# Kernel tuning notes

Hardware: AMD Instinct MI355X
Metric: run time of the kernel (lower is better)

The kernel has to match this reference:

```python
import jax, jax.numpy as jnp
import numpy as np

T, H, I, E, K = 2048, 1024, 768, 16, 4

def setup_inputs() -> dict:
    key = jax.random.key(0)
    k1, k2, k3, k4, k5 = jax.random.split(key, 5)
    hidden_states = jax.random.normal(k1, (T, H), dtype=jnp.float32)
    top_k_index = jax.random.randint(k2, (T, K), 0, E, dtype=jnp.int64)
    top_k_weights = jax.random.uniform(k3, (T, K), dtype=jnp.float32)
    gate_up_proj = jax.random.normal(k4, (E, 2 * I, H), dtype=jnp.float32) * 0.02
    down_proj = jax.random.normal(k5, (E, H, I), dtype=jnp.float32) * 0.02
    return {"hidden_states": hidden_states, "top_k_index": top_k_index,
            "top_k_weights": top_k_weights, "gate_up_proj": gate_up_proj,
            "down_proj": down_proj}

def reference(hidden_states, top_k_index, top_k_weights, gate_up_proj, down_proj):
    # Masked dense MoE: scan over experts, each expert does full-token GEMMs
    # and a per-token combine weight (sum of routing weights where routed to e).
    # index_add over token_idx == sum over k of (mask * weight) * expert_out.
    n_experts = gate_up_proj.shape[0]

    def body(acc, xs):
        w_gu, w_d, e = xs  # [2I,H], [H,I], scalar
        gu = hidden_states @ w_gu.T                 # [T, 2I]
        gate, up = jnp.split(gu, 2, axis=-1)        # [T, I] each
        h = jax.nn.silu(gate) * up                  # [T, I]
        out = h @ w_d.T                             # [T, H]
        w_tok = jnp.sum(jnp.where(top_k_index == e, top_k_weights, 0.0), axis=-1)  # [T]
        return acc + out * w_tok[:, None], None

    acc0 = jnp.zeros_like(hidden_states)
    final, _ = jax.lax.scan(body, acc0, (gate_up_proj, down_proj, jnp.arange(n_experts)))
    return final
```

## Files before the change

kernel.cpp:

```cpp
#include <hip/hip_runtime.h>
#include <hip/hip_bf16.h>
#include <stdint.h>

#define T_TOK 2048
#define H_DIM 1024
#define I_DIM 768
#define E_NUM 16
#define K_TOP 4
#define NSLOT (T_TOK * K_TOP)
#define PSLOT 10240
#define NTILE 80

typedef short  s16x8 __attribute__((ext_vector_type(8)));
typedef float  f32x4 __attribute__((ext_vector_type(4)));
typedef unsigned short u16x8 __attribute__((ext_vector_type(8)));

#define MEMFENCE asm volatile("" ::: "memory")

__device__ __forceinline__ void gload16(const void* g, void* l) {
  __builtin_amdgcn_global_load_lds(
      (const __attribute__((address_space(1))) uint32_t*)g,
      (__attribute__((address_space(3))) uint32_t*)l, 16, 0, 0);
}

__device__ __forceinline__ unsigned short f2bf(float f) {
  __hip_bfloat16 h = __float2bfloat16(f);
  return *reinterpret_cast<unsigned short*>(&h);
}

__device__ __forceinline__ void write_b_row(char* bregion, int r, int half,
                                            f32x4 f0, f32x4 f1, f32x4 f2, f32x4 f3) {
  u16x8 c0, c1;
  c0[0]=f2bf(f0[0]); c0[1]=f2bf(f0[1]); c0[2]=f2bf(f0[2]); c0[3]=f2bf(f0[3]);
  c0[4]=f2bf(f1[0]); c0[5]=f2bf(f1[1]); c0[6]=f2bf(f1[2]); c0[7]=f2bf(f1[3]);
  c1[0]=f2bf(f2[0]); c1[1]=f2bf(f2[1]); c1[2]=f2bf(f2[2]); c1[3]=f2bf(f2[3]);
  c1[4]=f2bf(f3[0]); c1[5]=f2bf(f3[1]); c1[6]=f2bf(f3[2]); c1[7]=f2bf(f3[3]);
  int xr = (r >> 1) & 3;
  char* wb = bregion + r * 64;
  *(u16x8*)(wb + (((2*half + 0) ^ xr) * 16)) = c0;
  *(u16x8*)(wb + (((2*half + 1) ^ xr) * 16)) = c1;
}

__global__ __launch_bounds__(256) void cvt_bf16_kernel(
    const float* __restrict__ in, unsigned short* __restrict__ out, int n8) {
  int i = blockIdx.x * 256 + threadIdx.x;
  if (i >= n8) return;
  const float4* p = (const float4*)in;
  float4 a = p[2 * (size_t)i];
  float4 b = p[2 * (size_t)i + 1];
  u16x8 o;
  o[0] = f2bf(a.x); o[1] = f2bf(a.y); o[2] = f2bf(a.z); o[3] = f2bf(a.w);
  o[4] = f2bf(b.x); o[5] = f2bf(b.y); o[6] = f2bf(b.z); o[7] = f2bf(b.w);
  *(u16x8*)(out + (size_t)i * 8) = o;
}

__global__ __launch_bounds__(256) void route_kernel(
    const int* __restrict__ idx, const float* __restrict__ wts,
    int* __restrict__ slot_tok, float* __restrict__ slot_w,
    int* __restrict__ slot_of, int* __restrict__ tile_expert) {
  __shared__ int cnt[256][16];
  __shared__ int tot[16];
  __shared__ int pb[17];
  int tid = threadIdx.x;

  for (int e = 0; e < 16; ++e) cnt[tid][e] = 0;
  const int s0 = tid * 32;
  for (int i = 0; i < 32; ++i) {
    int e = idx[s0 + i] & 15;
    cnt[tid][e]++;
  }
  __syncthreads();
  if (tid < 16) {
    int run = 0;
    for (int c = 0; c < 256; ++c) { int v = cnt[c][tid]; cnt[c][tid] = run; run += v; }
    tot[tid] = run;
  }
  __syncthreads();
  if (tid == 0) {
    int acc = 0;
    for (int e = 0; e < 16; ++e) { pb[e] = acc; acc += (tot[e] + 127) & ~127; }
    pb[16] = acc;
  }
  __syncthreads();
  for (int p = tid; p < PSLOT; p += 256) { slot_tok[p] = 0; slot_w[p] = 0.0f; }
  if (tid < NTILE) {
    int ef = -1;
    for (int e = 0; e < 16; ++e)
      if (tid * 128 >= pb[e] && tid * 128 < pb[e + 1]) ef = e;
    tile_expert[tid] = ef;
  }
  __syncthreads();
  for (int i = 0; i < 32; ++i) {
    int s = s0 + i;
    int e = idx[s] & 15;
    int pos = pb[e] + cnt[tid][e]++;
    slot_tok[pos] = s >> 2;
    slot_w[pos]   = wts[s];
    slot_of[s]    = pos;
  }
}


__global__ __launch_bounds__(256) void gemm1_kernel(
    const unsigned short* __restrict__ Xbf,
    const float* __restrict__ Wgu,
    const int* __restrict__ slot_tok,
    const int* __restrict__ tile_expert,
    unsigned short* __restrict__ hbuf) {
  int bid  = blockIdx.y * 12 + blockIdx.x;
  int sbid = (bid & 7) * 120 + (bid >> 3);
  int by   = sbid / 12;
  int bx   = sbid % 12;
  int e = tile_expert[by];
  if (e < 0) return;
  int m0 = by * 128;
  int tid = threadIdx.x;
  int lane = tid & 63, w = tid >> 6;
  int wr = w >> 1, wc = w & 1;

  __shared__ short lds[2 * 8192];
  char* buf0 = (char*)lds;
  char* buf1 = buf0 + 16384;

  int srow = tid >> 2;
  int swzc = ((tid & 3) ^ ((tid >> 3) & 3)) * 16;
  int tok0 = slot_tok[m0 + srow];
  int tok1 = slot_tok[m0 + 64 + srow];
  const char* gA0 = (const char*)(Xbf + (size_t)tok0 * H_DIM) + swzc;
  const char* gA1 = (const char*)(Xbf + (size_t)tok1 * H_DIM) + swzc;

  int brow = tid >> 1;
  int half = tid & 1;
  int prow = (brow < 64) ? (bx * 64 + brow) : (768 + bx * 64 + (brow - 64));
  const float* gB = Wgu + ((size_t)e * 1536 + prow) * H_DIM + half * 16;

  int pswz = ((lane >> 4) ^ (((lane & 15) >> 1) & 3)) * 8;

  f32x4 accg[4][2] = {};
  f32x4 accu[4][2] = {};
  f32x4 s0_0, s0_1, s0_2, s0_3, s1_0, s1_1, s1_2, s1_3;
  f32x4 s2_0, s2_1, s2_2, s2_3, s3_0, s3_1, s3_2, s3_3;

#define NT1 32
#define A_GLOAD1(kt, bufp) do {                               \
    int kk_ = (kt) < NT1 ? (kt) : NT1 - 1;                    \
    int ko_ = kk_ * 64;                                       \
    gload16(gA0 + ko_, (bufp) + tid * 16);                    \
    gload16(gA1 + ko_, (bufp) + 4096 + tid * 16);             \
  } while (0)
#define B_LOAD1(v0, v1, v2, v3, kt) do {                      \
    int kk_ = (kt) < NT1 ? (kt) : NT1 - 1;                    \
    const f32x4* p_ = (const f32x4*)(gB + (size_t)kk_ * 32);  \
    v0 = p_[0]; v1 = p_[1]; v2 = p_[2]; v3 = p_[3];           \
  } while (0)

#define G1_COMPUTE(bufp) do {                                                          \
    const short* La = (const short*)(bufp);                                            \
    s16x8 af[4], bgf[2], buf2[2];                                                      \
    _Pragma("unroll")                                                                  \
    for (int mi = 0; mi < 4; ++mi)                                                     \
      af[mi] = *(const s16x8*)(La + (wr * 64 + mi * 16 + (lane & 15)) * 32 + pswz);    \
    _Pragma("unroll")                                                                  \
    for (int ni = 0; ni < 2; ++ni) {                                                   \
      int row = wc * 32 + ni * 16 + (lane & 15);                                       \
      bgf[ni]  = *(const s16x8*)(La + 4096 + row * 32 + pswz);                         \
      buf2[ni] = *(const s16x8*)(La + 6144 + row * 32 + pswz);                         \
    }                                                                                  \
    _Pragma("unroll")                                                                  \
    for (int mi = 0; mi < 4; ++mi)                                                     \
      _Pragma("unroll")                                                                \
      for (int ni = 0; ni < 2; ++ni) {                                                 \
        accg[mi][ni] = __builtin_amdgcn_mfma_f32_16x16x32_bf16(af[mi], bgf[ni],  accg[mi][ni], 0, 0, 0); \
        accu[mi][ni] = __builtin_amdgcn_mfma_f32_16x16x32_bf16(af[mi], buf2[ni], accu[mi][ni], 0, 0, 0); \
      }                                                                                \
  } while (0)

#define ITER1(kt, wv0, wv1, wv2, wv3, lv0, lv1, lv2, lv3) do {  \
    char* cbuf_ = ((kt) & 1) ? buf1 : buf0;                     \
    char* nbuf_ = ((kt) & 1) ? buf0 : buf1;                     \
    MEMFENCE;                                                   \
    A_GLOAD1((kt) + 1, nbuf_);                                  \
    MEMFENCE;                                                   \
    B_LOAD1(lv0, lv1, lv2, lv3, (kt) + 3);                      \
    asm volatile("s_waitcnt vmcnt(10)" ::: "memory");           \
    write_b_row(nbuf_ + 8192, brow, half, wv0, wv1, wv2, wv3);  \
    asm volatile("s_waitcnt lgkmcnt(0)" ::: "memory");          \
    __builtin_amdgcn_s_barrier();                               \
    MEMFENCE;                                                   \
    G1_COMPUTE(cbuf_);                                          \
    MEMFENCE;                                                   \
    __builtin_amdgcn_s_barrier();                               \
  } while (0)

  A_GLOAD1(0, buf0);
  MEMFENCE;
  B_LOAD1(s0_0, s0_1, s0_2, s0_3, 0);
  MEMFENCE;
  B_LOAD1(s1_0, s1_1, s1_2, s1_3, 1);
  MEMFENCE;
  B_LOAD1(s2_0, s2_1, s2_2, s2_3, 2);
  asm volatile("s_waitcnt vmcnt(8)" ::: "memory");
  write_b_row(buf0 + 8192, brow, half, s0_0, s0_1, s0_2, s0_3);

  for (int kt = 0; kt < NT1; kt += 4) {
    ITER1(kt + 0, s1_0, s1_1, s1_2, s1_3, s3_0, s3_1, s3_2, s3_3);
    ITER1(kt + 1, s2_0, s2_1, s2_2, s2_3, s0_0, s0_1, s0_2, s0_3);
    ITER1(kt + 2, s3_0, s3_1, s3_2, s3_3, s1_0, s1_1, s1_2, s1_3);
    ITER1(kt + 3, s0_0, s0_1, s0_2, s0_3, s2_0, s2_1, s2_2, s2_3);
  }
#undef ITER1
#undef G1_COMPUTE
#undef B_LOAD1
#undef A_GLOAD1

#pragma unroll
  for (int mi = 0; mi < 4; ++mi) {
#pragma unroll
    for (int ni = 0; ni < 2; ++ni) {
      int col = bx * 64 + wc * 32 + ni * 16 + (lane & 15);
#pragma unroll
      for (int q = 0; q < 4; ++q) {
        int m = m0 + wr * 64 + mi * 16 + (lane >> 4) * 4 + q;
        float g = accg[mi][ni][q];
        float u = accu[mi][ni][q];
        float s = g / (1.0f + __expf(-g));
        hbuf[(size_t)m * I_DIM + col] = f2bf(s * u);
      }
    }
  }
}

__global__ __launch_bounds__(256) void gemm2_kernel(
    const unsigned short* __restrict__ hbuf,
    const float* __restrict__ Wd,
    const int* __restrict__ slot_tok,
    const float* __restrict__ slot_w,
    const int* __restrict__ tile_expert,
    float* __restrict__ y) {
  int bid  = blockIdx.y * 8 + blockIdx.x;
  int sbid = (bid & 7) * 80 + (bid >> 3);
  int by   = sbid >> 3;
  int bx   = sbid & 7;
  int e = tile_expert[by];
  if (e < 0) return;
  int m0 = by * 128;
  int tid = threadIdx.x;
  int lane = tid & 63, w = tid >> 6;
  int wr = w >> 1, wc = w & 1;

  __shared__ short lds[2 * 8192];
  char* buf0 = (char*)lds;
  char* buf1 = buf0 + 16384;

  int srow = tid >> 2;
  int swzc = ((tid & 3) ^ ((tid >> 3) & 3)) * 16;
  const char* gA0 = (const char*)(hbuf + (size_t)(m0 + srow) * I_DIM) + swzc;
  const char* gA1 = (const char*)(hbuf + (size_t)(m0 + 64 + srow) * I_DIM) + swzc;

  int brow = tid >> 1;
  int half = tid & 1;
  const float* gB = Wd + ((size_t)e * 1024 + bx * 128 + brow) * I_DIM + half * 16;

  int pswz = ((lane >> 4) ^ (((lane & 15) >> 1) & 3)) * 8;

  f32x4 acc[4][4] = {};
  f32x4 s0_0, s0_1, s0_2, s0_3, s1_0, s1_1, s1_2, s1_3;
  f32x4 s2_0, s2_1, s2_2, s2_3, s3_0, s3_1, s3_2, s3_3;

#define NT2 24
#define A_GLOAD2(kt, bufp) do {                               \
    int kk_ = (kt) < NT2 ? (kt) : NT2 - 1;                    \
    int ko_ = kk_ * 64;                                       \
    gload16(gA0 + ko_, (bufp) + tid * 16);                    \
    gload16(gA1 + ko_, (bufp) + 4096 + tid * 16);             \
  } while (0)
#define B_LOAD2(v0, v1, v2, v3, kt) do {                      \
    int kk_ = (kt) < NT2 ? (kt) : NT2 - 1;                    \
    const f32x4* p_ = (const f32x4*)(gB + (size_t)kk_ * 32);  \
    v0 = p_[0]; v1 = p_[1]; v2 = p_[2]; v3 = p_[3];           \
  } while (0)

#define G2_COMPUTE(bufp) do {                                                          \
    const short* La = (const short*)(bufp);                                            \
    s16x8 af[4], bf[4];                                                                \
    _Pragma("unroll")                                                                  \
    for (int mi = 0; mi < 4; ++mi)                                                     \
      af[mi] = *(const s16x8*)(La + (wr * 64 + mi * 16 + (lane & 15)) * 32 + pswz);    \
    _Pragma("unroll")                                                                  \
    for (int ni = 0; ni < 4; ++ni)                                                     \
      bf[ni] = *(const s16x8*)(La + 4096 + (wc * 64 + ni * 16 + (lane & 15)) * 32 + pswz); \
    _Pragma("unroll")                                                                  \
    for (int mi = 0; mi < 4; ++mi)                                                     \
      _Pragma("unroll")                                                                \
      for (int ni = 0; ni < 4; ++ni)                                                   \
        acc[mi][ni] = __builtin_amdgcn_mfma_f32_16x16x32_bf16(af[mi], bf[ni], acc[mi][ni], 0, 0, 0); \
  } while (0)

#define ITER2(kt, wv0, wv1, wv2, wv3, lv0, lv1, lv2, lv3) do {  \
    char* cbuf_ = ((kt) & 1) ? buf1 : buf0;                     \
    char* nbuf_ = ((kt) & 1) ? buf0 : buf1;                     \
    MEMFENCE;                                                   \
    A_GLOAD2((kt) + 1, nbuf_);                                  \
    MEMFENCE;                                                   \
    B_LOAD2(lv0, lv1, lv2, lv3, (kt) + 3);                      \
    asm volatile("s_waitcnt vmcnt(10)" ::: "memory");           \
    write_b_row(nbuf_ + 8192, brow, half, wv0, wv1, wv2, wv3);  \
    asm volatile("s_waitcnt lgkmcnt(0)" ::: "memory");          \
    __builtin_amdgcn_s_barrier();                               \
    MEMFENCE;                                                   \
    G2_COMPUTE(cbuf_);                                          \
    MEMFENCE;                                                   \
    __builtin_amdgcn_s_barrier();                               \
  } while (0)

  A_GLOAD2(0, buf0);
  MEMFENCE;
  B_LOAD2(s0_0, s0_1, s0_2, s0_3, 0);
  MEMFENCE;
  B_LOAD2(s1_0, s1_1, s1_2, s1_3, 1);
  MEMFENCE;
  B_LOAD2(s2_0, s2_1, s2_2, s2_3, 2);
  asm volatile("s_waitcnt vmcnt(8)" ::: "memory");
  write_b_row(buf0 + 8192, brow, half, s0_0, s0_1, s0_2, s0_3);

  for (int kt = 0; kt < NT2; kt += 4) {
    ITER2(kt + 0, s1_0, s1_1, s1_2, s1_3, s3_0, s3_1, s3_2, s3_3);
    ITER2(kt + 1, s2_0, s2_1, s2_2, s2_3, s0_0, s0_1, s0_2, s0_3);
    ITER2(kt + 2, s3_0, s3_1, s3_2, s3_3, s1_0, s1_1, s1_2, s1_3);
    ITER2(kt + 3, s0_0, s0_1, s0_2, s0_3, s2_0, s2_1, s2_2, s2_3);
  }
#undef ITER2
#undef G2_COMPUTE
#undef B_LOAD2
#undef A_GLOAD2

#pragma unroll
  for (int mi = 0; mi < 4; ++mi) {
#pragma unroll
    for (int q = 0; q < 4; ++q) {
      int m = m0 + wr * 64 + mi * 16 + (lane >> 4) * 4 + q;
      float wgt = slot_w[m];
      float* orow = y + (size_t)m * H_DIM + bx * 128 + wc * 64 + (lane & 15);
#pragma unroll
      for (int ni = 0; ni < 4; ++ni)
        orow[ni * 16] = acc[mi][ni][q] * wgt;
    }
  }
}

__global__ __launch_bounds__(256) void combine_kernel(
    const float* __restrict__ y, const int* __restrict__ slot_of,
    float* __restrict__ out) {
  int t = blockIdx.x;
  int c = threadIdx.x * 4;
  int s0 = slot_of[t * 4 + 0], s1 = slot_of[t * 4 + 1];
  int s2 = slot_of[t * 4 + 2], s3 = slot_of[t * 4 + 3];
  f32x4 v0 = *(const f32x4*)(y + (size_t)s0 * H_DIM + c);
  f32x4 v1 = *(const f32x4*)(y + (size_t)s1 * H_DIM + c);
  f32x4 v2 = *(const f32x4*)(y + (size_t)s2 * H_DIM + c);
  f32x4 v3 = *(const f32x4*)(y + (size_t)s3 * H_DIM + c);
  f32x4 r = (v0 + v1) + (v2 + v3);
  *(f32x4*)(out + (size_t)t * H_DIM + c) = r;
}

extern "C" void kernel_launch(void* const* d_in, const int* in_sizes, int n_in,
                              void* d_out, int out_size, void* d_ws, size_t ws_size,
                              hipStream_t stream) {
  const float* hs       = (const float*)d_in[0];
  const int*   topk_idx = (const int*)d_in[1];
  const float* topk_w   = (const float*)d_in[2];
  const float* w_gu     = (const float*)d_in[3];
  const float* w_d      = (const float*)d_in[4];
  float* out = (float*)d_out;

  char* ws = (char*)d_ws;
  unsigned short* Xbf  = (unsigned short*)(ws);
  unsigned short* hbuf = (unsigned short*)(ws + 4194304);
  float*          y    = (float*)(ws + 19922944);
  int*   slot_tok    = (int*)(ws + 61865984);
  float* slot_w      = (float*)(ws + 61906944);
  int*   slot_of     = (int*)(ws + 61947904);
  int*   tile_expert = (int*)(ws + 61980672);

  cvt_bf16_kernel<<<1024, 256, 0, stream>>>(hs, Xbf, T_TOK * H_DIM / 8);
  route_kernel<<<1, 256, 0, stream>>>(topk_idx, topk_w, slot_tok, slot_w, slot_of, tile_expert);

  gemm1_kernel<<<dim3(12, NTILE), 256, 0, stream>>>(Xbf, w_gu, slot_tok, tile_expert, hbuf);
  gemm2_kernel<<<dim3(8, NTILE), 256, 0, stream>>>(hbuf, w_d, slot_tok, slot_w, tile_expert, y);
  combine_kernel<<<T_TOK, 256, 0, stream>>>(y, slot_of, out);
}
```

Before: 135.4 us.

## Stage fp32 gate/up weights directly into LDS via async loads in gemm1

The gemm1 B operand (fp32 expert weights) is no longer loaded into registers and converted before an LDS write. It is now streamed with global_load_lds straight into a swizzled fp32 LDS tile and converted to bf16 at fragment read time. This replaces the register-staged 4-deep B pipeline with a simple double buffer where all A and B loads are asynchronous, and adds s_setprio around the MFMA block. It doubles LDS per block and repeats the fp32-to-bf16 conversion for each wave reading a fragment, which may reduce occupancy and add ALU work.

```diff
diff --git a/kernel.cpp b/kernel.cpp
--- a/kernel.cpp
+++ b/kernel.cpp
@@ -99,7 +99,6 @@
     slot_of[s]    = pos;
   }
 }
-
 
 __global__ __launch_bounds__(256) void gemm1_kernel(
     const unsigned short* __restrict__ Xbf,
@@ -114,113 +113,114 @@
   int e = tile_expert[by];
   if (e < 0) return;
   int m0 = by * 128;
-  int tid = threadIdx.x;
-  int lane = tid & 63, w = tid >> 6;
+  int t = threadIdx.x;
+  int lane = t & 63, w = t >> 6;
   int wr = w >> 1, wc = w & 1;
-
-  __shared__ short lds[2 * 8192];
-  char* buf0 = (char*)lds;
-  char* buf1 = buf0 + 16384;
-
-  int srow = tid >> 2;
-  int swzc = ((tid & 3) ^ ((tid >> 3) & 3)) * 16;
-  int tok0 = slot_tok[m0 + srow];
-  int tok1 = slot_tok[m0 + 64 + srow];
-  const char* gA0 = (const char*)(Xbf + (size_t)tok0 * H_DIM) + swzc;
-  const char* gA1 = (const char*)(Xbf + (size_t)tok1 * H_DIM) + swzc;
-
-  int brow = tid >> 1;
-  int half = tid & 1;
-  int prow = (brow < 64) ? (bx * 64 + brow) : (768 + bx * 64 + (brow - 64));
-  const float* gB = Wgu + ((size_t)e * 1536 + prow) * H_DIM + half * 16;
-
-  int pswz = ((lane >> 4) ^ (((lane & 15) >> 1) & 3)) * 8;
+  int l15 = lane & 15, lhi = lane >> 4;
+
+  __shared__ char lds[2 * 24576];
+  char* buf0 = lds;
+  char* buf1 = lds + 24576;
+
+  int arow = t >> 2;
+  int aswz = ((t & 3) ^ ((t >> 3) & 3)) * 16;
+  int tok0 = slot_tok[m0 + arow];
+  int tok1 = slot_tok[m0 + 64 + arow];
+  const char* gA0 = (const char*)(Xbf + (size_t)tok0 * H_DIM) + aswz;
+  const char* gA1 = (const char*)(Xbf + (size_t)tok1 * H_DIM) + aswz;
+
+  const char* gBs[4];
+#pragma unroll
+  for (int c = 0; c < 4; ++c) {
+    int r = c * 32 + (t >> 3);
+    int prow = (r < 64) ? (bx * 64 + r) : (768 + bx * 64 + (r - 64));
+    int q = (t & 7) ^ (r & 7);
+    gBs[c] = (const char*)(Wgu + ((size_t)e * 1536 + prow) * H_DIM) + q * 16;
+  }
+
+  int pswz = (lhi ^ ((l15 >> 1) & 3)) * 8;
 
   f32x4 accg[4][2] = {};
   f32x4 accu[4][2] = {};
-  f32x4 s0_0, s0_1, s0_2, s0_3, s1_0, s1_1, s1_2, s1_3;
-  f32x4 s2_0, s2_1, s2_2, s2_3, s3_0, s3_1, s3_2, s3_3;
 
 #define NT1 32
-#define A_GLOAD1(kt, bufp) do {                               \
-    int kk_ = (kt) < NT1 ? (kt) : NT1 - 1;                    \
-    int ko_ = kk_ * 64;                                       \
-    gload16(gA0 + ko_, (bufp) + tid * 16);                    \
-    gload16(gA1 + ko_, (bufp) + 4096 + tid * 16);             \
-  } while (0)
-#define B_LOAD1(v0, v1, v2, v3, kt) do {                      \
-    int kk_ = (kt) < NT1 ? (kt) : NT1 - 1;                    \
-    const f32x4* p_ = (const f32x4*)(gB + (size_t)kk_ * 32);  \
-    v0 = p_[0]; v1 = p_[1]; v2 = p_[2]; v3 = p_[3];           \
-  } while (0)
-
-#define G1_COMPUTE(bufp) do {                                                          \
-    const short* La = (const short*)(bufp);                                            \
-    s16x8 af[4], bgf[2], buf2[2];                                                      \
+#define G1_STAGE(bufp, kt) do {                               \
+    size_t ao = (size_t)(kt) * 64;                            \
+    size_t bo = (size_t)(kt) * 128;                           \
+    gload16(gA0 + ao, (bufp) + t * 16);                       \
+    gload16(gA1 + ao, (bufp) + 4096 + t * 16);                \
+    gload16(gBs[0] + bo, (bufp) + 8192 + t * 16);             \
+    gload16(gBs[1] + bo, (bufp) + 12288 + t * 16);            \
+    gload16(gBs[2] + bo, (bufp) + 16384 + t * 16);            \
+    gload16(gBs[3] + bo, (bufp) + 20480 + t * 16);            \
+  } while (0)
+
+#define B_FRAG(dst, cb, rb) do {                                              \
+    const char* base_ = (cb) + 8192 + (rb) * 128;                             \
+    f32x4 x0_ = *(const f32x4*)(base_ + (((2*lhi    ) ^ ((rb) & 7)) * 16));   \
+    f32x4 x1_ = *(const f32x4*)(base_ + (((2*lhi + 1) ^ ((rb) & 7)) * 16));   \
+    s16x8 o_;                                                                 \
+    o_[0]=(short)f2bf(x0_[0]); o_[1]=(short)f2bf(x0_[1]);                     \
+    o_[2]=(short)f2bf(x0_[2]); o_[3]=(short)f2bf(x0_[3]);                     \
+    o_[4]=(short)f2bf(x1_[0]); o_[5]=(short)f2bf(x1_[1]);                     \
+    o_[6]=(short)f2bf(x1_[2]); o_[7]=(short)f2bf(x1_[3]);                     \
+    dst = o_;                                                                 \
+  } while (0)
+
+#define G1_COMPUTE(cb) do {                                                            \
+    const short* La = (const short*)(cb);                                              \
+    s16x8 af[4], bg[2], bu[2];                                                         \
     _Pragma("unroll")                                                                  \
     for (int mi = 0; mi < 4; ++mi)                                                     \
-      af[mi] = *(const s16x8*)(La + (wr * 64 + mi * 16 + (lane & 15)) * 32 + pswz);    \
+      af[mi] = *(const s16x8*)(La + (wr * 64 + mi * 16 + l15) * 32 + pswz);            \
     _Pragma("unroll")                                                                  \
     for (int ni = 0; ni < 2; ++ni) {                                                   \
-      int row = wc * 32 + ni * 16 + (lane & 15);                                       \
-      bgf[ni]  = *(const s16x8*)(La + 4096 + row * 32 + pswz);                         \
-      buf2[ni] = *(const s16x8*)(La + 6144 + row * 32 + pswz);                         \
+      int rbg = wc * 32 + ni * 16 + l15;                                               \
+      B_FRAG(bg[ni], (cb), rbg);                                                       \
+      B_FRAG(bu[ni], (cb), rbg + 64);                                                  \
     }                                                                                  \
+    __builtin_amdgcn_s_setprio(1);                                                     \
     _Pragma("unroll")                                                                  \
     for (int mi = 0; mi < 4; ++mi)                                                     \
       _Pragma("unroll")                                                                \
       for (int ni = 0; ni < 2; ++ni) {                                                 \
-        accg[mi][ni] = __builtin_amdgcn_mfma_f32_16x16x32_bf16(af[mi], bgf[ni],  accg[mi][ni], 0, 0, 0); \
-        accu[mi][ni] = __builtin_amdgcn_mfma_f32_16x16x32_bf16(af[mi], buf2[ni], accu[mi][ni], 0, 0, 0); \
+        accg[mi][ni] = __builtin_amdgcn_mfma_f32_16x16x32_bf16(af[mi], bg[ni], accg[mi][ni], 0, 0, 0); \
+        accu[mi][ni] = __builtin_amdgcn_mfma_f32_16x16x32_bf16(af[mi], bu[ni], accu[mi][ni], 0, 0, 0); \
       }                                                                                \
-  } while (0)
-
-#define ITER1(kt, wv0, wv1, wv2, wv3, lv0, lv1, lv2, lv3) do {  \
-    char* cbuf_ = ((kt) & 1) ? buf1 : buf0;                     \
-    char* nbuf_ = ((kt) & 1) ? buf0 : buf1;                     \
-    MEMFENCE;                                                   \
-    A_GLOAD1((kt) + 1, nbuf_);                                  \
-    MEMFENCE;                                                   \
-    B_LOAD1(lv0, lv1, lv2, lv3, (kt) + 3);                      \
-    asm volatile("s_waitcnt vmcnt(10)" ::: "memory");           \
-    write_b_row(nbuf_ + 8192, brow, half, wv0, wv1, wv2, wv3);  \
-    asm volatile("s_waitcnt lgkmcnt(0)" ::: "memory");          \
-    __builtin_amdgcn_s_barrier();                               \
-    MEMFENCE;                                                   \
-    G1_COMPUTE(cbuf_);                                          \
-    MEMFENCE;                                                   \
-    __builtin_amdgcn_s_barrier();                               \
-  } while (0)
-
-  A_GLOAD1(0, buf0);
-  MEMFENCE;
-  B_LOAD1(s0_0, s0_1, s0_2, s0_3, 0);
-  MEMFENCE;
-  B_LOAD1(s1_0, s1_1, s1_2, s1_3, 1);
-  MEMFENCE;
-  B_LOAD1(s2_0, s2_1, s2_2, s2_3, 2);
-  asm volatile("s_waitcnt vmcnt(8)" ::: "memory");
-  write_b_row(buf0 + 8192, brow, half, s0_0, s0_1, s0_2, s0_3);
-
-  for (int kt = 0; kt < NT1; kt += 4) {
-    ITER1(kt + 0, s1_0, s1_1, s1_2, s1_3, s3_0, s3_1, s3_2, s3_3);
-    ITER1(kt + 1, s2_0, s2_1, s2_2, s2_3, s0_0, s0_1, s0_2, s0_3);
-    ITER1(kt + 2, s3_0, s3_1, s3_2, s3_3, s1_0, s1_1, s1_2, s1_3);
-    ITER1(kt + 3, s0_0, s0_1, s0_2, s0_3, s2_0, s2_1, s2_2, s2_3);
-  }
-#undef ITER1
+    __builtin_amdgcn_s_setprio(0);                                                     \
+  } while (0)
+
+  G1_STAGE(buf0, 0);
+  int cur = 0;
+  for (int kt = 0; kt < NT1; ++kt) {
+    char* cbuf = cur ? buf1 : buf0;
+    char* nbuf = cur ? buf0 : buf1;
+    if (kt + 1 < NT1) {
+      MEMFENCE;
+      G1_STAGE(nbuf, kt + 1);
+      asm volatile("s_waitcnt vmcnt(6)" ::: "memory");
+    } else {
+      asm volatile("s_waitcnt vmcnt(0)" ::: "memory");
+    }
+    __builtin_amdgcn_s_barrier();
+    MEMFENCE;
+    G1_COMPUTE(cbuf);
+    MEMFENCE;
+    __builtin_amdgcn_s_barrier();
+    cur ^= 1;
+  }
+#undef G1_STAGE
 #undef G1_COMPUTE
-#undef B_LOAD1
-#undef A_GLOAD1
+#undef B_FRAG
 
 #pragma unroll
   for (int mi = 0; mi < 4; ++mi) {
 #pragma unroll
     for (int ni = 0; ni < 2; ++ni) {
-      int col = bx * 64 + wc * 32 + ni * 16 + (lane & 15);
+      int col = bx * 64 + wc * 32 + ni * 16 + l15;
 #pragma unroll
       for (int q = 0; q < 4; ++q) {
-        int m = m0 + wr * 64 + mi * 16 + (lane >> 4) * 4 + q;
+        int m = m0 + wr * 64 + mi * 16 + lhi * 4 + q;
         float g = accg[mi][ni][q];
         float u = accu[mi][ni][q];
         float s = g / (1.0f + __expf(-g));
@@ -383,7 +383,8 @@
   int*   tile_expert = (int*)(ws + 61980672);
 
   cvt_bf16_kernel<<<1024, 256, 0, stream>>>(hs, Xbf, T_TOK * H_DIM / 8);
-  route_kernel<<<1, 256, 0, stream>>>(topk_idx, topk_w, slot_tok, slot_w, slot_of, tile_expert);
+  route_kernel<<<1, 256, 0, stream>>>(topk_idx, topk_w, slot_tok, slot_w,
+                                      slot_of, tile_expert);
 
   gemm1_kernel<<<dim3(12, NTILE), 256, 0, stream>>>(Xbf, w_gu, slot_tok, tile_expert, hbuf);
   gemm2_kernel<<<dim3(8, NTILE), 256, 0, stream>>>(hbuf, w_d, slot_tok, slot_w, tile_expert, y);
```

Result: faster. 127.2 us (-6.1%).
